# Optimization experiments

Hardware: AMD Instinct MI355X
Metric: run time of the kernel (lower is better)

The kernel has to match this reference:

```python
import jax, jax.numpy as jnp
import numpy as np

B, N, E, D_IN, D_OUT = 8, 8192, 131072, 128, 128
LN_EPS = 1e-5

def setup_inputs() -> dict:
    key = jax.random.key(0)
    k1, k2, k3, k4 = jax.random.split(key, 4)
    node_features = jax.random.normal(k1, (B, N, D_IN), dtype=jnp.float32)
    edge_index = jax.random.randint(k2, (B, 2, E), 0, N, dtype=jnp.int64)
    node_mask = jnp.ones((B, N), dtype=jnp.float32)
    # Linear params (torch Linear: y = x @ W.T + b)
    W = jax.random.normal(k3, (D_OUT, D_IN), dtype=jnp.float32) / np.sqrt(D_IN)
    b = jax.random.normal(k4, (D_OUT,), dtype=jnp.float32) * 0.01
    # LayerNorm params
    gamma = jnp.ones((D_OUT,), dtype=jnp.float32)
    beta = jnp.zeros((D_OUT,), dtype=jnp.float32)
    return {"node_features": node_features, "edge_index": edge_index,
            "node_mask": node_mask, "W": W, "b": b, "gamma": gamma, "beta": beta}

def reference(node_features, edge_index, node_mask, W, b, gamma, beta):
    max_nodes = node_features.shape[1]
    h = jnp.einsum('bni,oi->bno', node_features, W) + b  # [B,N,D_OUT]
    def agg_one(hb, eb):
        # gather source features then scatter-add into targets
        return jax.ops.segment_sum(hb[eb[0]], eb[1], num_segments=max_nodes)
    aggregated = jax.vmap(agg_one)(h, edge_index)  # [B,N,D_OUT]
    h = h + aggregated / jnp.sqrt(jnp.float32(max_nodes))
    # dropout is identity in eval mode
    mu = jnp.mean(h, axis=-1, keepdims=True)
    var = jnp.mean((h - mu) ** 2, axis=-1, keepdims=True)
    h = (h - mu) * jax.lax.rsqrt(var + LN_EPS) * gamma + beta
    h = jax.nn.relu(h)
    return h * node_mask[..., None]
```

## Files before the change

### kernel.cpp

```cpp
#include <hip/hip_runtime.h>

#define B_ 8
#define N_ 8192
#define E_ 131072
#define D_ 128
#define M_ (B_ * N_)
#define SLOTS 64
constexpr float INV_SQRT_N = 0.011048543456039806f;
constexpr float LN_EPS_C = 1e-5f;

typedef __attribute__((ext_vector_type(8))) short bf16x8;
typedef __attribute__((ext_vector_type(4))) float f32x4;
typedef __attribute__((ext_vector_type(4))) float f32x4v;
typedef __attribute__((ext_vector_type(4))) unsigned u32x4;

static __device__ __forceinline__ unsigned short f2bf(float f) {
  unsigned u = __float_as_uint(f);
  u += 0x7fffu + ((u >> 16) & 1u);
  return (unsigned short)(u >> 16);
}
static __device__ __forceinline__ float bflo(unsigned u) {
  return __uint_as_float(u << 16);
}
static __device__ __forceinline__ float bfhi(unsigned u) {
  return __uint_as_float(u & 0xffff0000u);
}
static __device__ __forceinline__ bf16x8 cvt8v(const f32x4v a, const f32x4v b) {
  bf16x8 r;
  r[0] = (short)f2bf(a.x); r[1] = (short)f2bf(a.y);
  r[2] = (short)f2bf(a.z); r[3] = (short)f2bf(a.w);
  r[4] = (short)f2bf(b.x); r[5] = (short)f2bf(b.y);
  r[6] = (short)f2bf(b.z); r[7] = (short)f2bf(b.w);
  return r;
}

__global__ __launch_bounds__(256, 4) void gemm_fill_kernel(
    const float* __restrict__ X, const float* __restrict__ W,
    const float* __restrict__ bias, const int* __restrict__ eidx,
    int* __restrict__ cnt, unsigned short* __restrict__ bucket,
    unsigned short* __restrict__ hb) {
  if (blockIdx.x < 256) {
    const int wave = threadIdx.x >> 6;
    const int lane = threadIdx.x & 63;
    const int m16 = lane & 15;
    const int q = lane >> 4;
    const int hf = wave & 1;
    const int ng = wave >> 1;

    bf16x8 wf[4][4];
#pragma unroll
    for (int kt4 = 0; kt4 < 4; ++kt4) {
#pragma unroll
      for (int tt = 0; tt < 4; ++tt) {
        const float* wr = W + (size_t)(hf * 64 + tt * 16 + m16) * D_ +
                          kt4 * 32 + q * 8;
        wf[kt4][tt] = cvt8v(*(const f32x4v*)wr, *(const f32x4v*)(wr + 4));
      }
    }

    const int nbase0 = blockIdx.x * 256 + ng * 128;
#pragma unroll 2
    for (int s = 0; s < 8; ++s) {
      const int nbase = nbase0 + s * 16;
      const float* xrow = X + (size_t)(nbase + m16) * D_;

      f32x4 acc[4];
#pragma unroll
      for (int tt = 0; tt < 4; ++tt) acc[tt] = (f32x4){0.f, 0.f, 0.f, 0.f};

#pragma unroll
      for (int kt4 = 0; kt4 < 4; ++kt4) {
        const f32x4v xa = __builtin_nontemporal_load(
            (const f32x4v*)(xrow + kt4 * 32 + q * 8));
        const f32x4v xb = __builtin_nontemporal_load(
            (const f32x4v*)(xrow + kt4 * 32 + q * 8 + 4));
        const bf16x8 xf = cvt8v(xa, xb);
#pragma unroll
        for (int tt = 0; tt < 4; ++tt) {
          acc[tt] = __builtin_amdgcn_mfma_f32_16x16x32_bf16(wf[kt4][tt], xf,
                                                            acc[tt], 0, 0, 0);
        }
      }

      const size_t orow = (size_t)(nbase + m16) * D_;
#pragma unroll
      for (int tt = 0; tt < 4; ++tt) {
        const int f0 = hf * 64 + tt * 16 + q * 4;
        const float4 b4 = *(const float4*)&bias[f0];
        uint2 uu;
        uu.x = (unsigned)f2bf(acc[tt][0] + b4.x) |
               ((unsigned)f2bf(acc[tt][1] + b4.y) << 16);
        uu.y = (unsigned)f2bf(acc[tt][2] + b4.z) |
               ((unsigned)f2bf(acc[tt][3] + b4.w) << 16);
        *(uint2*)(hb + orow + f0) = uu;
      }
    }
  } else {
    const int f = blockIdx.x - 256;
    const int batch = f & 7;
    const int chunk = f >> 3;
    const int base = batch * 2 * E_;
    const int e0 = chunk * 1024 + threadIdx.x * 4;
    const int4 sv = *(const int4*)&eidx[base + e0];
    const int4 tv = *(const int4*)&eidx[base + E_ + e0];
    const int nb = batch << 13;
    const int n0 = nb + tv.x, n1 = nb + tv.y, n2 = nb + tv.z, n3 = nb + tv.w;
    const int p0 = atomicAdd(&cnt[n0], 1);
    const int p1 = atomicAdd(&cnt[n1], 1);
    const int p2 = atomicAdd(&cnt[n2], 1);
    const int p3 = atomicAdd(&cnt[n3], 1);
    if (p0 < SLOTS) bucket[(size_t)n0 * SLOTS + p0] = (unsigned short)sv.x;
    if (p1 < SLOTS) bucket[(size_t)n1 * SLOTS + p1] = (unsigned short)sv.y;
    if (p2 < SLOTS) bucket[(size_t)n2 * SLOTS + p2] = (unsigned short)sv.z;
    if (p3 < SLOTS) bucket[(size_t)n3 * SLOTS + p3] = (unsigned short)sv.w;
  }
}

__global__ __launch_bounds__(256, 8) void gather_finalize_kernel(
    const unsigned short* __restrict__ hb, const unsigned short* __restrict__ bucket,
    const int* __restrict__ cnt, const float* __restrict__ mask,
    const float* __restrict__ gamma, const float* __restrict__ beta,
    float* __restrict__ out) {
  const int bid = blockIdx.x;
  const int batch = bid & 7;
  const int wave = threadIdx.x >> 6;
  const int lane = threadIdx.x & 63;
  const int g = lane >> 4;
  const int c = lane & 15;
  const int r = (bid >> 3) * 16 + wave * 4 + g;
  const int row = batch * N_ + r;

  const u32x4* hub4 = (const u32x4*)hb + (size_t)batch * N_ * 16;

  const int deg = min(cnt[row], SLOTS);
  const uint2 su = *(const uint2*)&bucket[(size_t)row * SLOTS + c * 4];
  const u32x4 ur = hub4[r * 16 + c];
  const float m = mask[row];

  float a[8];
#pragma unroll
  for (int k = 0; k < 8; ++k) a[k] = 0.f;

  int jb = 0;
  for (; jb + 8 <= deg; jb += 8) {
    const int L = jb >> 2;
    const unsigned w0 = (unsigned)__shfl((int)su.x, L, 16);
    const unsigned w1 = (unsigned)__shfl((int)su.y, L, 16);
    const unsigned w2 = (unsigned)__shfl((int)su.x, L + 1, 16);
    const unsigned w3 = (unsigned)__shfl((int)su.y, L + 1, 16);
    const int idx[8] = {(int)(w0 & 0xffff), (int)(w0 >> 16),
                        (int)(w1 & 0xffff), (int)(w1 >> 16),
                        (int)(w2 & 0xffff), (int)(w2 >> 16),
                        (int)(w3 & 0xffff), (int)(w3 >> 16)};
    u32x4 v[8];
#pragma unroll
    for (int i = 0; i < 8; ++i) v[i] = hub4[idx[i] * 16 + c];
#pragma unroll
    for (int i = 0; i < 8; ++i) {
      a[0] += bflo(v[i].x); a[1] += bfhi(v[i].x);
      a[2] += bflo(v[i].y); a[3] += bfhi(v[i].y);
      a[4] += bflo(v[i].z); a[5] += bfhi(v[i].z);
      a[6] += bflo(v[i].w); a[7] += bfhi(v[i].w);
    }
  }
  for (; jb < deg; ++jb) {
    const int L = jb >> 2;
    const unsigned w = ((jb >> 1) & 1) ? (unsigned)__shfl((int)su.y, L, 16)
                                       : (unsigned)__shfl((int)su.x, L, 16);
    const int idx = (jb & 1) ? (int)(w >> 16) : (int)(w & 0xffff);
    const u32x4 v = hub4[idx * 16 + c];
    a[0] += bflo(v.x); a[1] += bfhi(v.x);
    a[2] += bflo(v.y); a[3] += bfhi(v.y);
    a[4] += bflo(v.z); a[5] += bfhi(v.z);
    a[6] += bflo(v.w); a[7] += bfhi(v.w);
  }

  float x[8];
  x[0] = bflo(ur.x) + a[0] * INV_SQRT_N;
  x[1] = bfhi(ur.x) + a[1] * INV_SQRT_N;
  x[2] = bflo(ur.y) + a[2] * INV_SQRT_N;
  x[3] = bfhi(ur.y) + a[3] * INV_SQRT_N;
  x[4] = bflo(ur.z) + a[4] * INV_SQRT_N;
  x[5] = bfhi(ur.z) + a[5] * INV_SQRT_N;
  x[6] = bflo(ur.w) + a[6] * INV_SQRT_N;
  x[7] = bfhi(ur.w) + a[7] * INV_SQRT_N;

  float s0 = 0.f, ss = 0.f;
#pragma unroll
  for (int k = 0; k < 8; ++k) {
    s0 += x[k];
    ss += x[k] * x[k];
  }
#pragma unroll
  for (int o = 8; o >= 1; o >>= 1) {
    s0 += __shfl_xor(s0, o, 16);
    ss += __shfl_xor(ss, o, 16);
  }
  const float mu = s0 * (1.f / 128.f);
  float var = ss * (1.f / 128.f) - mu * mu;
  var = var < 0.f ? 0.f : var;
  const float rstd = rsqrtf(var + LN_EPS_C);

  const f32x4v g0 = *((const f32x4v*)gamma + c * 2);
  const f32x4v g1 = *((const f32x4v*)gamma + c * 2 + 1);
  const f32x4v b0 = *((const f32x4v*)beta + c * 2);
  const f32x4v b1 = *((const f32x4v*)beta + c * 2 + 1);

  f32x4v o0, o1;
  o0.x = (x[0] - mu) * rstd * g0.x + b0.x;
  o0.y = (x[1] - mu) * rstd * g0.y + b0.y;
  o0.z = (x[2] - mu) * rstd * g0.z + b0.z;
  o0.w = (x[3] - mu) * rstd * g0.w + b0.w;
  o1.x = (x[4] - mu) * rstd * g1.x + b1.x;
  o1.y = (x[5] - mu) * rstd * g1.y + b1.y;
  o1.z = (x[6] - mu) * rstd * g1.z + b1.z;
  o1.w = (x[7] - mu) * rstd * g1.w + b1.w;
  o0.x = (o0.x > 0.f ? o0.x : 0.f) * m;
  o0.y = (o0.y > 0.f ? o0.y : 0.f) * m;
  o0.z = (o0.z > 0.f ? o0.z : 0.f) * m;
  o0.w = (o0.w > 0.f ? o0.w : 0.f) * m;
  o1.x = (o1.x > 0.f ? o1.x : 0.f) * m;
  o1.y = (o1.y > 0.f ? o1.y : 0.f) * m;
  o1.z = (o1.z > 0.f ? o1.z : 0.f) * m;
  o1.w = (o1.w > 0.f ? o1.w : 0.f) * m;

  f32x4v* op = (f32x4v*)out + (size_t)row * 32 + c * 2;
  __builtin_nontemporal_store(o0, op);
  __builtin_nontemporal_store(o1, op + 1);
}

extern "C" void kernel_launch(void* const* d_in, const int* in_sizes, int n_in,
                              void* d_out, int out_size, void* d_ws,
                              size_t ws_size, hipStream_t stream) {
  const float* X = (const float*)d_in[0];
  const int* eidx = (const int*)d_in[1];
  const float* mask = (const float*)d_in[2];
  const float* W = (const float*)d_in[3];
  const float* bias = (const float*)d_in[4];
  const float* gamma = (const float*)d_in[5];
  const float* beta = (const float*)d_in[6];
  float* out = (float*)d_out;

  unsigned short* hb = (unsigned short*)d_ws;
  unsigned short* bucket = hb + (size_t)M_ * D_;
  int* cnt = (int*)(bucket + (size_t)M_ * SLOTS);

  (void)hipMemsetAsync(cnt, 0, (size_t)M_ * sizeof(int), stream);

  gemm_fill_kernel<<<256 + 1024, 256, 0, stream>>>(X, W, bias, eidx, cnt,
                                                   bucket, hb);
  gather_finalize_kernel<<<M_ / 16, 256, 0, stream>>>(hb, bucket, cnt, mask,
                                                      gamma, beta, out);
}
```

Measured before the change: 183.0 us.

## Bin edges per node window in LDS instead of global atomics

Replaces the global-atomic edge bucketing with per-block windows of 256 target nodes, where each block scans all edges of its batch and bins matching ones using shared-memory atomics, then copies counts and buckets to global memory coalesced. This removes the count memset and the scattered global atomics and stores. In exchange each batch's edge list is re-read once per window, and the fill kernel's larger shared memory footprint can reduce occupancy for the GEMM blocks.

```diff
diff --git a/kernel.cpp b/kernel.cpp
--- a/kernel.cpp
+++ b/kernel.cpp
@@ -6,6 +6,8 @@
 #define D_ 128
 #define M_ (B_ * N_)
 #define SLOTS 64
+#define WIN 256
+#define NWIN (N_ / WIN)
 constexpr float INV_SQRT_N = 0.011048543456039806f;
 constexpr float LN_EPS_C = 1e-5f;
 
@@ -39,6 +41,8 @@
     const float* __restrict__ bias, const int* __restrict__ eidx,
     int* __restrict__ cnt, unsigned short* __restrict__ bucket,
     unsigned short* __restrict__ hb) {
+  __shared__ unsigned cnt_l[WIN];
+  __shared__ unsigned short bkt_l[WIN * SLOTS];
   if (blockIdx.x < 256) {
     const int wave = threadIdx.x >> 6;
     const int lane = threadIdx.x & 63;
@@ -98,21 +102,44 @@
   } else {
     const int f = blockIdx.x - 256;
     const int batch = f & 7;
-    const int chunk = f >> 3;
-    const int base = batch * 2 * E_;
-    const int e0 = chunk * 1024 + threadIdx.x * 4;
-    const int4 sv = *(const int4*)&eidx[base + e0];
-    const int4 tv = *(const int4*)&eidx[base + E_ + e0];
-    const int nb = batch << 13;
-    const int n0 = nb + tv.x, n1 = nb + tv.y, n2 = nb + tv.z, n3 = nb + tv.w;
-    const int p0 = atomicAdd(&cnt[n0], 1);
-    const int p1 = atomicAdd(&cnt[n1], 1);
-    const int p2 = atomicAdd(&cnt[n2], 1);
-    const int p3 = atomicAdd(&cnt[n3], 1);
-    if (p0 < SLOTS) bucket[(size_t)n0 * SLOTS + p0] = (unsigned short)sv.x;
-    if (p1 < SLOTS) bucket[(size_t)n1 * SLOTS + p1] = (unsigned short)sv.y;
-    if (p2 < SLOTS) bucket[(size_t)n2 * SLOTS + p2] = (unsigned short)sv.z;
-    if (p3 < SLOTS) bucket[(size_t)n3 * SLOTS + p3] = (unsigned short)sv.w;
+    const int w = f >> 3;
+    const int t = threadIdx.x;
+
+    cnt_l[t] = 0u;
+    __syncthreads();
+
+    const int* __restrict__ srcp = eidx + batch * 2 * E_;
+    const int* __restrict__ tgtp = srcp + E_;
+    const int wbase = w * WIN;
+
+#pragma unroll 2
+    for (int it = 0; it < E_ / 1024; ++it) {
+      const int e = it * 1024 + t * 4;
+      const int4 tv = *(const int4*)&tgtp[e];
+      const int4 sv = *(const int4*)&srcp[e];
+      const unsigned l0 = (unsigned)(tv.x - wbase);
+      const unsigned l1 = (unsigned)(tv.y - wbase);
+      const unsigned l2 = (unsigned)(tv.z - wbase);
+      const unsigned l3 = (unsigned)(tv.w - wbase);
+      unsigned p0 = SLOTS, p1 = SLOTS, p2 = SLOTS, p3 = SLOTS;
+      if (l0 < WIN) p0 = atomicAdd(&cnt_l[l0], 1u);
+      if (l1 < WIN) p1 = atomicAdd(&cnt_l[l1], 1u);
+      if (l2 < WIN) p2 = atomicAdd(&cnt_l[l2], 1u);
+      if (l3 < WIN) p3 = atomicAdd(&cnt_l[l3], 1u);
+      if (p0 < SLOTS) bkt_l[l0 * SLOTS + p0] = (unsigned short)sv.x;
+      if (p1 < SLOTS) bkt_l[l1 * SLOTS + p1] = (unsigned short)sv.y;
+      if (p2 < SLOTS) bkt_l[l2 * SLOTS + p2] = (unsigned short)sv.z;
+      if (p3 < SLOTS) bkt_l[l3 * SLOTS + p3] = (unsigned short)sv.w;
+    }
+    __syncthreads();
+
+    const int nodebase = batch * N_ + wbase;
+    cnt[nodebase + t] = (int)cnt_l[t];
+    const u32x4* ls = (const u32x4*)bkt_l;
+    u32x4* gd = (u32x4*)(bucket + (size_t)nodebase * SLOTS);
+#pragma unroll
+    for (int i = 0; i < (WIN * SLOTS * 2) / (16 * 256); ++i)
+      gd[i * 256 + t] = ls[i * 256 + t];
   }
 }
 
@@ -245,10 +272,9 @@
   unsigned short* bucket = hb + (size_t)M_ * D_;
   int* cnt = (int*)(bucket + (size_t)M_ * SLOTS);
 
-  (void)hipMemsetAsync(cnt, 0, (size_t)M_ * sizeof(int), stream);
-
-  gemm_fill_kernel<<<256 + 1024, 256, 0, stream>>>(X, W, bias, eidx, cnt,
-                                                   bucket, hb);
+
+  gemm_fill_kernel<<<256 + 256, 256, 0, stream>>>(X, W, bias, eidx, cnt,
+                                                  bucket, hb);
   gather_finalize_kernel<<<M_ / 16, 256, 0, stream>>>(hb, bucket, cnt, mask,
                                                       gamma, beta, out);
 }
```

Measured after the change: 185.6 us. About the same (+1.4%).

## Replace global-atomic edge bucketing with LDS histogram counting sort

Applied to the files above, without the earlier changes.

Replaces per-edge global atomicAdd bucketing with a three-phase counting sort. Each block histograms its edge chunk in shared memory, a prefix kernel scans the per-chunk counts, and a place kernel writes sources into deterministic slots using LDS atomics. The output buffer is reused as scratch for the chunk histograms, and the memset is removed. The aim is to avoid contended global atomics, at the cost of two extra launches, 32 KB of LDS per block (lower occupancy), and extra reads of the edge list.

```diff
diff --git a/kernel.cpp b/kernel.cpp
--- a/kernel.cpp
+++ b/kernel.cpp
@@ -6,6 +6,8 @@
 #define D_ 128
 #define M_ (B_ * N_)
 #define SLOTS 64
+#define NCH 32
+#define CHE (E_ / NCH)
 constexpr float INV_SQRT_N = 0.011048543456039806f;
 constexpr float LN_EPS_C = 1e-5f;
 
@@ -34,11 +36,11 @@
   return r;
 }
 
-__global__ __launch_bounds__(256, 4) void gemm_fill_kernel(
+__global__ __launch_bounds__(256, 2) void gemm_count_kernel(
     const float* __restrict__ X, const float* __restrict__ W,
     const float* __restrict__ bias, const int* __restrict__ eidx,
-    int* __restrict__ cnt, unsigned short* __restrict__ bucket,
-    unsigned short* __restrict__ hb) {
+    unsigned short* __restrict__ histc, unsigned short* __restrict__ hb) {
+  __shared__ unsigned hist[N_];
   if (blockIdx.x < 256) {
     const int wave = threadIdx.x >> 6;
     const int lane = threadIdx.x & 63;
@@ -58,7 +60,8 @@
       }
     }
 
-    const int nbase0 = blockIdx.x * 256 + ng * 128;
+    const int bi = blockIdx.x;
+    const int nbase0 = (bi & 7) * N_ + (bi >> 3) * 256 + ng * 128;
 #pragma unroll 2
     for (int s = 0; s < 8; ++s) {
       const int nbase = nbase0 + s * 16;
@@ -97,22 +100,88 @@
     }
   } else {
     const int f = blockIdx.x - 256;
-    const int batch = f & 7;
-    const int chunk = f >> 3;
-    const int base = batch * 2 * E_;
-    const int e0 = chunk * 1024 + threadIdx.x * 4;
-    const int4 sv = *(const int4*)&eidx[base + e0];
-    const int4 tv = *(const int4*)&eidx[base + E_ + e0];
-    const int nb = batch << 13;
-    const int n0 = nb + tv.x, n1 = nb + tv.y, n2 = nb + tv.z, n3 = nb + tv.w;
-    const int p0 = atomicAdd(&cnt[n0], 1);
-    const int p1 = atomicAdd(&cnt[n1], 1);
-    const int p2 = atomicAdd(&cnt[n2], 1);
-    const int p3 = atomicAdd(&cnt[n3], 1);
-    if (p0 < SLOTS) bucket[(size_t)n0 * SLOTS + p0] = (unsigned short)sv.x;
-    if (p1 < SLOTS) bucket[(size_t)n1 * SLOTS + p1] = (unsigned short)sv.y;
-    if (p2 < SLOTS) bucket[(size_t)n2 * SLOTS + p2] = (unsigned short)sv.z;
-    if (p3 < SLOTS) bucket[(size_t)n3 * SLOTS + p3] = (unsigned short)sv.w;
+    const int b = f & 7;
+    const int c = f >> 3;
+    const int t = threadIdx.x;
+
+#pragma unroll
+    for (int i = 0; i < N_ / 256; ++i) hist[t + i * 256] = 0u;
+    __syncthreads();
+
+    const int* __restrict__ tgtp = eidx + b * 2 * E_ + E_ + c * CHE;
+#pragma unroll
+    for (int k = 0; k < 4; ++k) {
+      const int4 tv = *(const int4*)(tgtp + t * 16 + k * 4);
+      atomicAdd(&hist[tv.x], 1u);
+      atomicAdd(&hist[tv.y], 1u);
+      atomicAdd(&hist[tv.z], 1u);
+      atomicAdd(&hist[tv.w], 1u);
+    }
+    __syncthreads();
+
+    unsigned* dst = (unsigned*)(histc + ((size_t)b * NCH + c) * N_);
+#pragma unroll
+    for (int i = 0; i < N_ / 512; ++i) {
+      const int j = t + i * 256;
+      const unsigned lo = hist[2 * j];
+      const unsigned hi = hist[2 * j + 1];
+      dst[j] = (lo & 0xffffu) | (hi << 16);
+    }
+  }
+}
+
+__global__ __launch_bounds__(256, 8) void prefix_kernel(
+    unsigned short* __restrict__ histc, int* __restrict__ cnt) {
+  const int b = blockIdx.x & 7;
+  const int nb = blockIdx.x >> 3;
+  const int n = nb * 256 + threadIdx.x;
+  unsigned short* base = histc + (size_t)b * NCH * N_ + n;
+  unsigned short v[NCH];
+#pragma unroll
+  for (int c = 0; c < NCH; ++c) v[c] = base[(size_t)c * N_];
+  unsigned run = 0;
+#pragma unroll
+  for (int c = 0; c < NCH; ++c) {
+    const unsigned x = v[c];
+    base[(size_t)c * N_] = (unsigned short)run;
+    run += x;
+  }
+  cnt[b * N_ + n] = (int)run;
+}
+
+__global__ __launch_bounds__(256, 2) void place_kernel(
+    const int* __restrict__ eidx, const unsigned short* __restrict__ histc,
+    unsigned short* __restrict__ bucket) {
+  __shared__ unsigned hist[N_];
+  const int b = blockIdx.x & 7;
+  const int c = blockIdx.x >> 3;
+  const int t = threadIdx.x;
+
+#pragma unroll
+  for (int i = 0; i < N_ / 256; ++i) hist[t + i * 256] = 0u;
+  __syncthreads();
+
+  const int* __restrict__ srcp = eidx + b * 2 * E_ + c * CHE;
+  const int* __restrict__ tgtp = srcp + E_;
+  const unsigned short* __restrict__ basep = histc + ((size_t)b * NCH + c) * N_;
+  unsigned short* __restrict__ bkt = bucket + (size_t)b * N_ * SLOTS;
+
+#pragma unroll
+  for (int k = 0; k < 4; ++k) {
+    const int4 tv = *(const int4*)(tgtp + t * 16 + k * 4);
+    const int4 sv = *(const int4*)(srcp + t * 16 + k * 4);
+    const unsigned b0 = basep[tv.x];
+    const unsigned b1 = basep[tv.y];
+    const unsigned b2 = basep[tv.z];
+    const unsigned b3 = basep[tv.w];
+    const unsigned p0 = atomicAdd(&hist[tv.x], 1u) + b0;
+    const unsigned p1 = atomicAdd(&hist[tv.y], 1u) + b1;
+    const unsigned p2 = atomicAdd(&hist[tv.z], 1u) + b2;
+    const unsigned p3 = atomicAdd(&hist[tv.w], 1u) + b3;
+    if (p0 < SLOTS) bkt[(size_t)tv.x * SLOTS + p0] = (unsigned short)sv.x;
+    if (p1 < SLOTS) bkt[(size_t)tv.y * SLOTS + p1] = (unsigned short)sv.y;
+    if (p2 < SLOTS) bkt[(size_t)tv.z * SLOTS + p2] = (unsigned short)sv.z;
+    if (p3 < SLOTS) bkt[(size_t)tv.w * SLOTS + p3] = (unsigned short)sv.w;
   }
 }
 
@@ -244,11 +313,11 @@
   unsigned short* hb = (unsigned short*)d_ws;
   unsigned short* bucket = hb + (size_t)M_ * D_;
   int* cnt = (int*)(bucket + (size_t)M_ * SLOTS);
-
-  (void)hipMemsetAsync(cnt, 0, (size_t)M_ * sizeof(int), stream);
-
-  gemm_fill_kernel<<<256 + 1024, 256, 0, stream>>>(X, W, bias, eidx, cnt,
-                                                   bucket, hb);
+  unsigned short* histc = (unsigned short*)out;
+
+  gemm_count_kernel<<<512, 256, 0, stream>>>(X, W, bias, eidx, histc, hb);
+  prefix_kernel<<<256, 256, 0, stream>>>(histc, cnt);
+  place_kernel<<<256, 256, 0, stream>>>(eidx, histc, bucket);
   gather_finalize_kernel<<<M_ / 16, 256, 0, stream>>>(hb, bucket, cnt, mask,
                                                       gamma, beta, out);
 }
```

New measurement: 147.0 us. 1.24x faster.
